# Performance work log

Hardware: AMD Instinct MI355X
Metric: run time of the kernel (lower is better)

## Reference

```python
import jax, jax.numpy as jnp
import numpy as np

NEG_INF = jnp.float32(-1e9)  # finite large-negative avoids -inf*0 NaNs in grads


def setup_inputs() -> dict:
    key = jax.random.key(0)
    k1, k2, k3, k4, k5 = jax.random.split(key, 5)
    B, T, S, D = 16, 1024, 2048, 1024
    source = jax.random.normal(k1, (B, T, D), dtype=jnp.float32)
    memory_bank = jax.random.normal(k2, (B, S, D), dtype=jnp.float32)
    memory_lengths = jax.random.randint(k3, (B,), 1, S + 1, dtype=jnp.int32)
    # torch nn.Linear weights are [out_features, in_features]
    W_in = jax.random.normal(k4, (D, D), dtype=jnp.float32) / jnp.sqrt(jnp.float32(D))
    W_out = jax.random.normal(k5, (D, 2 * D), dtype=jnp.float32) / jnp.sqrt(jnp.float32(2 * D))
    return {"source": source, "memory_bank": memory_bank,
            "memory_lengths": memory_lengths, "W_in": W_in, "W_out": W_out}


def reference(source, memory_bank, memory_lengths, W_in, W_out):
    # GlobalAttention(attn_type='general', attn_func='softmax'), multi-step path
    B, T, D = source.shape
    S = memory_bank.shape[1]
    # score: general -> linear_in(h_t) @ h_s^T
    h_t = jnp.einsum('btd,ed->bte', source, W_in)            # [B,T,D]
    align = jnp.einsum('bte,bse->bts', h_t, memory_bank)      # [B,T,S]
    # sequence_mask on memory_lengths, broadcast over target dim
    mask = jnp.arange(S, dtype=jnp.int32)[None, None, :] < memory_lengths[:, None, None]
    align = jnp.where(mask, align, NEG_INF)
    align_vectors = jax.nn.softmax(align, axis=-1)            # [B,T,S]
    c = jnp.einsum('bts,bsd->btd', align_vectors, memory_bank)  # [B,T,D]
    concat_c = jnp.concatenate([c, source], axis=-1)          # [B,T,2D]
    attn_h = jnp.einsum('btf,of->bto', concat_c, W_out)       # linear_out, no bias for 'general'
    attn_h = jnp.tanh(attn_h)
    # not one_step -> transpose to [T,B,*]
    return attn_h.transpose(1, 0, 2), align_vectors.transpose(1, 0, 2)
```

## Files before the change

kernel.cpp:

```cpp
#include <hip/hip_runtime.h>

typedef __attribute__((ext_vector_type(8))) short s16x8;
typedef __attribute__((ext_vector_type(8))) _Float16 f16x8;
typedef __attribute__((ext_vector_type(4))) float f32x4;
typedef __attribute__((ext_vector_type(4))) unsigned short u16x4;
typedef unsigned short u16;

__device__ __forceinline__ u16 f2bf(float x) {
  unsigned u = __builtin_bit_cast(unsigned, x);
  u = u + 0x7fffu + ((u >> 16) & 1u);
  return (u16)(u >> 16);
}
__device__ __forceinline__ float bf2f(u16 h) {
  return __builtin_bit_cast(float, (unsigned)h << 16);
}
__device__ __forceinline__ void split_bf(float x, u16 &h, u16 &l) {
  h = f2bf(x); l = f2bf(x - bf2f(h));
}
__device__ __forceinline__ u16 f2h(float x) {
  return __builtin_bit_cast(u16, (_Float16)x);
}

typedef __attribute__((address_space(1))) const unsigned int as1c_u32;
typedef __attribute__((address_space(3))) unsigned int as3_u32;
__device__ __forceinline__ void gload16(const void* g, void* l) {
  __builtin_amdgcn_global_load_lds((as1c_u32*)g, (as3_u32*)l, 16, 0, 0);
}

__global__ __launch_bounds__(256) void split_copy_k(
    const float* __restrict__ in, u16* __restrict__ oh, u16* __restrict__ ol, long n4) {
  const long i = (long)blockIdx.x * 256 + threadIdx.x;
  if (i >= n4) return;
  const f32x4 v = *(const f32x4*)(in + i * 4);
  u16x4 h, l;
#pragma unroll
  for (int e = 0; e < 4; ++e) { u16 hh, ll; split_bf(v[e], hh, ll); h[e] = hh; l[e] = ll; }
  *(u16x4*)(oh + i * 4) = h;
  *(u16x4*)(ol + i * 4) = l;
}

__global__ __launch_bounds__(256) void copy_f16_k(
    const float* __restrict__ in, u16* __restrict__ oh, long n4) {
  const long i = (long)blockIdx.x * 256 + threadIdx.x;
  if (i >= n4) return;
  const f32x4 v = *(const f32x4*)(in + i * 4);
  u16x4 h;
#pragma unroll
  for (int e = 0; e < 4; ++e) h[e] = f2h(v[e]);
  *(u16x4*)(oh + i * 4) = h;
}

__global__ __launch_bounds__(256) void transpose_f16_k(
    const float* __restrict__ in, u16* __restrict__ oh) {
  __shared__ float tile[64][65];
  const int b = blockIdx.z;
  const int s0 = blockIdx.x * 64, d0 = blockIdx.y * 64;
  const float* pin = in + (long)b * 2048 * 1024;
  const int t = threadIdx.x;
#pragma unroll
  for (int i = 0; i < 16; ++i) {
    const int idx = i * 256 + t;
    const int r = idx >> 6, c = idx & 63;
    tile[r][c] = pin[(long)(s0 + r) * 1024 + d0 + c];
  }
  __syncthreads();
  u16* poh = oh + (long)b * 1024 * 2048;
#pragma unroll
  for (int i = 0; i < 16; ++i) {
    const int idx = i * 256 + t;
    const int r = idx >> 6, c = idx & 63;
    poh[(long)(d0 + r) * 2048 + s0 + c] = f2h(tile[c][r]);
  }
}

__global__ __launch_bounds__(256) void softmax_k(
    float* __restrict__ alignBuf, const int* __restrict__ lens, float* __restrict__ outP) {
  const int row = blockIdx.x;
  const int b = row >> 10;
  const int tt = row & 1023;
  const int len = lens[b];
  float* arow = alignBuf + (long)row * 2048;
  const int t = threadIdx.x;
  const int lane = t & 63, wv = t >> 6;
  float v[8];
  float mx = -3.0e38f;
#pragma unroll
  for (int j = 0; j < 8; ++j) {
    const int s = j * 256 + t;
    float x = arow[s];
    x = (s < len) ? x : -1.0e9f;
    v[j] = x;
    mx = fmaxf(mx, x);
  }
#pragma unroll
  for (int off = 32; off; off >>= 1) mx = fmaxf(mx, __shfl_xor(mx, off));
  __shared__ float redm[4], reds[4];
  if (lane == 0) redm[wv] = mx;
  __syncthreads();
  mx = fmaxf(fmaxf(redm[0], redm[1]), fmaxf(redm[2], redm[3]));
  float e[8]; float sum = 0.f;
#pragma unroll
  for (int j = 0; j < 8; ++j) { e[j] = __expf(v[j] - mx); sum += e[j]; }
#pragma unroll
  for (int off = 32; off; off >>= 1) sum += __shfl_xor(sum, off);
  if (lane == 0) reds[wv] = sum;
  __syncthreads();
  sum = reds[0] + reds[1] + reds[2] + reds[3];
  const float inv = 1.0f / sum;
  u16* ph = (u16*)arow;
  float* orow = outP + ((long)tt * 16 + b) * 2048;
#pragma unroll
  for (int j = 0; j < 8; ++j) {
    const int s = j * 256 + t;
    const float pv = e[j] * inv;
    orow[s] = pv;
    ph[s] = f2h(pv);
  }
}

template<int EP, int MASK>
__global__ __launch_bounds__(512) void gemmX(
    const u16* __restrict__ Ah, const u16* __restrict__ Al, int lda, long sA,
    const u16* __restrict__ Bh, const u16* __restrict__ Bl, int ldb, long sB,
    int K, const int* __restrict__ lens,
    float* __restrict__ Cf, u16* __restrict__ Ch, u16* __restrict__ Cl,
    int ldc, long sC, int lgx, int lgxy, int nwg) {
  __shared__ __align__(16) u16 ldsAh[8192];
  __shared__ __align__(16) u16 ldsAl[8192];
  __shared__ __align__(16) u16 ldsBh[4096];
  __shared__ __align__(16) u16 ldsBl[4096];

  const int orig = blockIdx.x;
  const int wg = (orig & 7) * (nwg >> 3) + (orig >> 3);
  const int bx = wg & ((1 << lgx) - 1);
  const int by = (wg >> lgx) & ((1 << (lgxy - lgx)) - 1);
  const int bz = wg >> lgxy;

  const long m0 = (long)by * 256;
  const long n0 = (long)bx * 128;

  if constexpr (MASK == 1) {
    if (n0 >= lens[bz]) return;
  }

  const u16* pAh = Ah + (long)bz * sA;
  const u16* pAl = Al + (long)bz * sA;
  const u16* pBh = Bh + (long)bz * sB;
  const u16* pBl = Bl + (long)bz * sB;

  const int t = threadIdx.x;
  const int lane = t & 63;
  const int wv = t >> 6;
  const int wm = wv >> 1;
  const int wn = wv & 1;
  const int lk = lane >> 4;
  const int lr = lane & 15;

  f32x4 acc[4][4];
#pragma unroll
  for (int i = 0; i < 4; ++i)
#pragma unroll
    for (int j = 0; j < 4; ++j) acc[i][j] = 0.0f;

  for (int k0 = 0; k0 < K; k0 += 32) {
    __syncthreads();
#pragma unroll
    for (int j = 0; j < 2; ++j) {
      const int ci = (j * 8 + wv) * 64;
      const int c = ci + lane;
      const int kc = c >> 8;
      const int r = c & 255;
      const long aoff = (m0 + r) * (long)lda + (k0 + kc * 8);
      gload16(pAh + aoff, &ldsAh[ci * 8]);
      gload16(pAl + aoff, &ldsAl[ci * 8]);
    }
    {
      const int ci = wv * 64;
      const int c = ci + lane;
      const int kc = c >> 7;
      const int r = c & 127;
      const long boff = (n0 + r) * (long)ldb + (k0 + kc * 8);
      gload16(pBh + boff, &ldsBh[ci * 8]);
      gload16(pBl + boff, &ldsBl[ci * 8]);
    }
    __syncthreads();

    s16x8 ah[4], al[4], bh[4], bl[4];
#pragma unroll
    for (int f = 0; f < 4; ++f) {
      const int ra = wm * 64 + f * 16 + lr;
      const int rb = wn * 64 + f * 16 + lr;
      ah[f] = *(const s16x8*)&ldsAh[(lk * 256 + ra) * 8];
      al[f] = *(const s16x8*)&ldsAl[(lk * 256 + ra) * 8];
      bh[f] = *(const s16x8*)&ldsBh[(lk * 128 + rb) * 8];
      bl[f] = *(const s16x8*)&ldsBl[(lk * 128 + rb) * 8];
    }
#pragma unroll
    for (int i = 0; i < 4; ++i)
#pragma unroll
      for (int j = 0; j < 4; ++j) {
        acc[i][j] = __builtin_amdgcn_mfma_f32_16x16x32_bf16(ah[i], bh[j], acc[i][j], 0, 0, 0);
        acc[i][j] = __builtin_amdgcn_mfma_f32_16x16x32_bf16(ah[i], bl[j], acc[i][j], 0, 0, 0);
        acc[i][j] = __builtin_amdgcn_mfma_f32_16x16x32_bf16(al[i], bh[j], acc[i][j], 0, 0, 0);
      }
  }

#pragma unroll
  for (int fm = 0; fm < 4; ++fm)
#pragma unroll
    for (int fn = 0; fn < 4; ++fn)
#pragma unroll
      for (int r = 0; r < 4; ++r) {
        const long row = m0 + wm * 64 + fm * 16 + (lane >> 4) * 4 + r;
        const long col = n0 + wn * 64 + fn * 16 + lr;
        const float v = acc[fm][fn][r];
        if constexpr (EP == 0) {
          Cf[(long)bz * sC + row * ldc + col] = v;
        } else {
          u16 h, l; split_bf(v, h, l);
          const long o = (long)bz * sC + row * ldc + col;
          Ch[o] = h; Cl[o] = l;
        }
      }
}

template<int EP, int MASK>
__global__ __launch_bounds__(512) void gemmW(
    const u16* __restrict__ A1, const u16* __restrict__ A2, int kSplitA, int lda, long sA,
    const u16* __restrict__ B, int ldb, long sB,
    int K, const int* __restrict__ lens,
    float* __restrict__ Cf, u16* __restrict__ Ch,
    int ldc, long sC, int lgx, int lgxy, int nwg) {
  __shared__ __align__(16) u16 ldsA[16384];
  __shared__ __align__(16) u16 ldsB[8192];

  const int orig = blockIdx.x;
  const int wg = (orig & 7) * (nwg >> 3) + (orig >> 3);
  const int bx = wg & ((1 << lgx) - 1);
  const int by = (wg >> lgx) & ((1 << (lgxy - lgx)) - 1);
  const int bz = wg >> lgxy;

  const long m0 = (long)by * 256;
  const long n0 = (long)bx * 128;

  int Klim = K;
  if constexpr (MASK == 2) {
    const int kl = (lens[bz] + 63) & ~63;
    Klim = kl < K ? kl : K;
  }

  const u16* pA1 = A1 + (long)bz * sA;
  const u16* pA2 = A2 + (long)bz * sA;
  const u16* pB  = B  + (long)bz * sB;

  const int t = threadIdx.x;
  const int lane = t & 63;
  const int wv = t >> 6;
  const int wm = wv >> 1;
  const int wn = wv & 1;
  const int lk = lane >> 4;
  const int lr = lane & 15;

  f32x4 acc[4][4];
#pragma unroll
  for (int i = 0; i < 4; ++i)
#pragma unroll
    for (int j = 0; j < 4; ++j) acc[i][j] = 0.0f;

  for (int k0 = 0; k0 < Klim; k0 += 64) {
    __syncthreads();
#pragma unroll
    for (int j = 0; j < 4; ++j) {
      const int ci = (j * 8 + wv) * 64;
      const int c = ci + lane;
      const int kc = c >> 8;
      const int r = c & 255;
      const int k = k0 + kc * 8;
      const u16* a = pA1; long ka = k;
      if (k >= kSplitA) { a = pA2; ka = k - kSplitA; }
      gload16(a + (m0 + r) * (long)lda + ka, &ldsA[ci * 8]);
    }
#pragma unroll
    for (int j = 0; j < 2; ++j) {
      const int ci = (j * 8 + wv) * 64;
      const int c = ci + lane;
      const int kc = c >> 7;
      const int r = c & 127;
      const int k = k0 + kc * 8;
      gload16(pB + (n0 + r) * (long)ldb + k, &ldsB[ci * 8]);
    }
    __syncthreads();

#pragma unroll
    for (int ks = 0; ks < 2; ++ks) {
      const int kc = ks * 4 + lk;
      f16x8 a[4], b[4];
#pragma unroll
      for (int f = 0; f < 4; ++f) {
        const int ra = wm * 64 + f * 16 + lr;
        const int rb = wn * 64 + f * 16 + lr;
        a[f] = *(const f16x8*)&ldsA[(kc * 256 + ra) * 8];
        b[f] = *(const f16x8*)&ldsB[(kc * 128 + rb) * 8];
      }
#pragma unroll
      for (int i = 0; i < 4; ++i)
#pragma unroll
        for (int j = 0; j < 4; ++j)
          acc[i][j] = __builtin_amdgcn_mfma_f32_16x16x32_f16(a[i], b[j], acc[i][j], 0, 0, 0);
    }
  }

#pragma unroll
  for (int fm = 0; fm < 4; ++fm)
#pragma unroll
    for (int fn = 0; fn < 4; ++fn)
#pragma unroll
      for (int r = 0; r < 4; ++r) {
        const long row = m0 + wm * 64 + fm * 16 + (lane >> 4) * 4 + r;
        const long col = n0 + wn * 64 + fn * 16 + lr;
        const float v = acc[fm][fn][r];
        if constexpr (EP == 2) {
          const long bb = row >> 10;
          const long tt = row & 1023;
          Cf[(tt * 16 + bb) * (long)ldc + col] = tanhf(v);
        } else {
          Ch[(long)bz * sC + row * ldc + col] = f2h(v);
        }
      }
}

extern "C" void kernel_launch(void* const* d_in, const int* in_sizes, int n_in,
                              void* d_out, int out_size, void* d_ws, size_t ws_size,
                              hipStream_t stream) {
  (void)in_sizes; (void)n_in; (void)out_size; (void)ws_size;
  const float* src = (const float*)d_in[0];
  const float* mb  = (const float*)d_in[1];
  const int*   lens= (const int*)d_in[2];
  const float* Wi  = (const float*)d_in[3];
  const float* Wo  = (const float*)d_in[4];
  float* out = (float*)d_out;

  char* p = (char*)d_ws;
  u16* mbS_hi  = (u16*)p;
  u16* mbS_lo  = (u16*)(p + (64L << 20));
  u16* srcU_hi = (u16*)(p + (128L << 20));
  u16* srcU_lo = (u16*)(p + (160L << 20));
  u16* htc_hi  = (u16*)(p + (192L << 20));
  u16* htc_lo  = (u16*)(p + (224L << 20));
  float* alignBuf = (float*)(p + (256L << 20));
  u16* Wi_hi = (u16*)alignBuf;
  u16* Wi_lo = Wi_hi + 1048576;
  u16* mbT    = mbS_lo;
  u16* Wo_f16 = mbS_hi;
  u16* srcF16 = mbS_hi + 2097152;

  dim3 blk(256);
  split_copy_k<<<dim3(32768), blk, 0, stream>>>(mb,  mbS_hi, mbS_lo, 8388608L);
  split_copy_k<<<dim3(16384), blk, 0, stream>>>(src, srcU_hi, srcU_lo, 4194304L);
  split_copy_k<<<dim3(1024),  blk, 0, stream>>>(Wi,  Wi_hi,  Wi_lo,  262144L);

  gemmX<1, 0><<<dim3(512), dim3(512), 0, stream>>>(
      srcU_hi, srcU_lo, 1024, 0L,
      Wi_hi, Wi_lo, 1024, 0L,
      1024, lens,
      nullptr, htc_hi, htc_lo, 1024, 0L,
      3, 9, 512);

  gemmX<0, 1><<<dim3(1024), dim3(512), 0, stream>>>(
      htc_hi, htc_lo, 1024, 1048576L,
      mbS_hi, mbS_lo, 1024, 2097152L,
      1024, lens,
      alignBuf, nullptr, nullptr, 2048, 2097152L,
      4, 6, 1024);

  softmax_k<<<dim3(16384), blk, 0, stream>>>(alignBuf, lens, out + 16777216L);

  transpose_f16_k<<<dim3(32, 16, 16), blk, 0, stream>>>(mb, mbT);
  copy_f16_k<<<dim3(2048),  blk, 0, stream>>>(Wo,  Wo_f16, 524288L);
  copy_f16_k<<<dim3(16384), blk, 0, stream>>>(src, srcF16, 4194304L);

  gemmW<3, 2><<<dim3(512), dim3(512), 0, stream>>>(
      (const u16*)alignBuf, (const u16*)alignBuf, 1 << 30, 4096, 4194304L,
      mbT, 2048, 2097152L,
      2048, lens,
      nullptr, htc_hi, 1024, 1048576L,
      3, 5, 512);

  gemmW<2, 0><<<dim3(512), dim3(512), 0, stream>>>(
      htc_hi, srcF16, 1024, 1024, 0L,
      Wo_f16, 2048, 0L,
      2048, lens,
      out, nullptr, 1024, 0L,
      3, 9, 512);
}
```

Baseline: 922.8 us.

## Fuse fp32-to-bf16 split of B operand into GEMM tile loads

Replaces the split-precision GEMM with a variant that reads the fp32 B operand (memory bank, W_in) directly and splits it into bf16 hi/lo while filling shared memory. This removes the separate split_copy passes over the 64M-element memory bank and W_in, along with their workspace writes and reads. The tile shrinks to 128x128 with 256 threads and two blocks per CU, and loads switch from async global-to-LDS copies to register-staged vector stores. The trade-off is redundant split work and twice the fp32 traffic per B tile, since each B tile is reloaded by every M-block. The softmax also skips loading masked elements.

```diff
diff --git a/kernel.cpp b/kernel.cpp
--- a/kernel.cpp
+++ b/kernel.cpp
@@ -1,6 +1,7 @@
 #include <hip/hip_runtime.h>
 
 typedef __attribute__((ext_vector_type(8))) short s16x8;
+typedef __attribute__((ext_vector_type(8))) unsigned short u16x8;
 typedef __attribute__((ext_vector_type(8))) _Float16 f16x8;
 typedef __attribute__((ext_vector_type(4))) float f32x4;
 typedef __attribute__((ext_vector_type(4))) unsigned short u16x4;
@@ -87,8 +88,7 @@
 #pragma unroll
   for (int j = 0; j < 8; ++j) {
     const int s = j * 256 + t;
-    float x = arow[s];
-    x = (s < len) ? x : -1.0e9f;
+    const float x = (s < len) ? arow[s] : -1.0e9f;
     v[j] = x;
     mx = fmaxf(mx, x);
   }
@@ -119,16 +119,14 @@
 }
 
 template<int EP, int MASK>
-__global__ __launch_bounds__(512) void gemmX(
+__global__ __launch_bounds__(256, 2) void gemmR(
     const u16* __restrict__ Ah, const u16* __restrict__ Al, int lda, long sA,
-    const u16* __restrict__ Bh, const u16* __restrict__ Bl, int ldb, long sB,
+    const float* __restrict__ Bf, int ldb, long sB,
     int K, const int* __restrict__ lens,
     float* __restrict__ Cf, u16* __restrict__ Ch, u16* __restrict__ Cl,
     int ldc, long sC, int lgx, int lgxy, int nwg) {
-  __shared__ __align__(16) u16 ldsAh[8192];
-  __shared__ __align__(16) u16 ldsAl[8192];
-  __shared__ __align__(16) u16 ldsBh[4096];
-  __shared__ __align__(16) u16 ldsBl[4096];
+  __shared__ __align__(16) u16 ldsA[2][4096];
+  __shared__ __align__(16) u16 ldsB[2][4096];
 
   const int orig = blockIdx.x;
   const int wg = (orig & 7) * (nwg >> 3) + (orig >> 3);
@@ -136,7 +134,7 @@
   const int by = (wg >> lgx) & ((1 << (lgxy - lgx)) - 1);
   const int bz = wg >> lgxy;
 
-  const long m0 = (long)by * 256;
+  const long m0 = (long)by * 128;
   const long n0 = (long)bx * 128;
 
   if constexpr (MASK == 1) {
@@ -145,8 +143,7 @@
 
   const u16* pAh = Ah + (long)bz * sA;
   const u16* pAl = Al + (long)bz * sA;
-  const u16* pBh = Bh + (long)bz * sB;
-  const u16* pBl = Bl + (long)bz * sB;
+  const float* pBf = Bf + (long)bz * sB;
 
   const int t = threadIdx.x;
   const int lane = t & 63;
@@ -155,6 +152,7 @@
   const int wn = wv & 1;
   const int lk = lane >> 4;
   const int lr = lane & 15;
+  const int fragBase = lk * 1024;
 
   f32x4 acc[4][4];
 #pragma unroll
@@ -166,22 +164,18 @@
     __syncthreads();
 #pragma unroll
     for (int j = 0; j < 2; ++j) {
-      const int ci = (j * 8 + wv) * 64;
-      const int c = ci + lane;
-      const int kc = c >> 8;
-      const int r = c & 255;
-      const long aoff = (m0 + r) * (long)lda + (k0 + kc * 8);
-      gload16(pAh + aoff, &ldsAh[ci * 8]);
-      gload16(pAl + aoff, &ldsAl[ci * 8]);
-    }
-    {
-      const int ci = wv * 64;
-      const int c = ci + lane;
-      const int kc = c >> 7;
-      const int r = c & 127;
-      const long boff = (n0 + r) * (long)ldb + (k0 + kc * 8);
-      gload16(pBh + boff, &ldsBh[ci * 8]);
-      gload16(pBl + boff, &ldsBl[ci * 8]);
+      const int c = j * 256 + t;
+      const int kc = c >> 7, r = c & 127;
+      const int k = k0 + kc * 8;
+      const long aoff = (m0 + r) * (long)lda + k;
+      *(u16x8*)&ldsA[0][c * 8] = *(const u16x8*)(pAh + aoff);
+      *(u16x8*)&ldsA[1][c * 8] = *(const u16x8*)(pAl + aoff);
+      const float* s = pBf + (n0 + r) * (long)ldb + k;
+      u16x8 bh, bl;
+#pragma unroll
+      for (int e = 0; e < 8; ++e) { u16 hh, ll; split_bf(s[e], hh, ll); bh[e] = hh; bl[e] = ll; }
+      *(u16x8*)&ldsB[0][c * 8] = bh;
+      *(u16x8*)&ldsB[1][c * 8] = bl;
     }
     __syncthreads();
 
@@ -190,10 +184,10 @@
     for (int f = 0; f < 4; ++f) {
       const int ra = wm * 64 + f * 16 + lr;
       const int rb = wn * 64 + f * 16 + lr;
-      ah[f] = *(const s16x8*)&ldsAh[(lk * 256 + ra) * 8];
-      al[f] = *(const s16x8*)&ldsAl[(lk * 256 + ra) * 8];
-      bh[f] = *(const s16x8*)&ldsBh[(lk * 128 + rb) * 8];
-      bl[f] = *(const s16x8*)&ldsBl[(lk * 128 + rb) * 8];
+      ah[f] = *(const s16x8*)&ldsA[0][fragBase + ra * 8];
+      al[f] = *(const s16x8*)&ldsA[1][fragBase + ra * 8];
+      bh[f] = *(const s16x8*)&ldsB[0][fragBase + rb * 8];
+      bl[f] = *(const s16x8*)&ldsB[1][fragBase + rb * 8];
     }
 #pragma unroll
     for (int i = 0; i < 4; ++i)
@@ -341,43 +335,40 @@
   float* out = (float*)d_out;
 
   char* p = (char*)d_ws;
-  u16* mbS_hi  = (u16*)p;
-  u16* mbS_lo  = (u16*)(p + (64L << 20));
-  u16* srcU_hi = (u16*)(p + (128L << 20));
-  u16* srcU_lo = (u16*)(p + (160L << 20));
-  u16* htc_hi  = (u16*)(p + (192L << 20));
-  u16* htc_lo  = (u16*)(p + (224L << 20));
-  float* alignBuf = (float*)(p + (256L << 20));
+  u16* srcU_hi = (u16*)p;
+  u16* srcU_lo = (u16*)(p + (32L << 20));
+  u16* htc_hi  = (u16*)(p + (64L << 20));
+  u16* htc_lo  = (u16*)(p + (96L << 20));
+  u16* srcF16  = (u16*)(p + (128L << 20));
+  u16* Wo_f16  = (u16*)(p + (160L << 20));
+  float* alignBuf = (float*)(p + (164L << 20));
   u16* Wi_hi = (u16*)alignBuf;
   u16* Wi_lo = Wi_hi + 1048576;
-  u16* mbT    = mbS_lo;
-  u16* Wo_f16 = mbS_hi;
-  u16* srcF16 = mbS_hi + 2097152;
+  u16* mbT   = srcU_hi;
 
   dim3 blk(256);
-  split_copy_k<<<dim3(32768), blk, 0, stream>>>(mb,  mbS_hi, mbS_lo, 8388608L);
   split_copy_k<<<dim3(16384), blk, 0, stream>>>(src, srcU_hi, srcU_lo, 4194304L);
-  split_copy_k<<<dim3(1024),  blk, 0, stream>>>(Wi,  Wi_hi,  Wi_lo,  262144L);
-
-  gemmX<1, 0><<<dim3(512), dim3(512), 0, stream>>>(
+  copy_f16_k<<<dim3(16384), blk, 0, stream>>>(src, srcF16, 4194304L);
+  copy_f16_k<<<dim3(2048),  blk, 0, stream>>>(Wo,  Wo_f16, 524288L);
+  (void)Wi_hi; (void)Wi_lo;
+
+  gemmR<1, 0><<<dim3(1024), blk, 0, stream>>>(
       srcU_hi, srcU_lo, 1024, 0L,
-      Wi_hi, Wi_lo, 1024, 0L,
+      Wi, 1024, 0L,
       1024, lens,
       nullptr, htc_hi, htc_lo, 1024, 0L,
-      3, 9, 512);
-
-  gemmX<0, 1><<<dim3(1024), dim3(512), 0, stream>>>(
+      3, 10, 1024);
+
+  gemmR<0, 1><<<dim3(2048), blk, 0, stream>>>(
       htc_hi, htc_lo, 1024, 1048576L,
-      mbS_hi, mbS_lo, 1024, 2097152L,
+      mb, 1024, 2097152L,
       1024, lens,
       alignBuf, nullptr, nullptr, 2048, 2097152L,
-      4, 6, 1024);
+      4, 7, 2048);
 
   softmax_k<<<dim3(16384), blk, 0, stream>>>(alignBuf, lens, out + 16777216L);
 
   transpose_f16_k<<<dim3(32, 16, 16), blk, 0, stream>>>(mb, mbT);
-  copy_f16_k<<<dim3(2048),  blk, 0, stream>>>(Wo,  Wo_f16, 524288L);
-  copy_f16_k<<<dim3(16384), blk, 0, stream>>>(src, srcF16, 4194304L);
 
   gemmW<3, 2><<<dim3(512), dim3(512), 0, stream>>>(
       (const u16*)alignBuf, (const u16*)alignBuf, 1 << 30, 4096, 4194304L,
```

After: 808.7 us. -12.4%, faster.
